# Kernel optimization log

Measured on AMD Instinct MI355X. Metric: run time of the kernel, lower is better.

## Reference

```python
import jax, jax.numpy as jnp
import numpy as np

E, D, H, F = 1024, 64, 16, 4096  # embedding, per-head dim, heads, mlp hidden
B, S = 2, 2048
EPS = 1e-5


def _layernorm(x, g, b):
    m = jnp.mean(x, axis=-1, keepdims=True)
    v = jnp.mean((x - m) ** 2, axis=-1, keepdims=True)
    return (x - m) * jax.lax.rsqrt(v + EPS) * g + b


def setup_inputs() -> dict:
    key = jax.random.key(0)
    ks = jax.random.split(key, 12)
    s_e = 1.0 / np.sqrt(E)
    s_f = 1.0 / np.sqrt(F)
    return {
        "x": jax.random.normal(ks[0], (B, S, E), jnp.float32),
        "Wq": jax.random.normal(ks[1], (H, E, D), jnp.float32) * s_e,
        "bq": jnp.zeros((H, D), jnp.float32),
        "Wk": jax.random.normal(ks[2], (H, E, D), jnp.float32) * s_e,
        "bk": jnp.zeros((H, D), jnp.float32),
        "Wv": jax.random.normal(ks[3], (H, E, D), jnp.float32) * s_e,
        "bv": jnp.zeros((H, D), jnp.float32),
        "Wo": jax.random.normal(ks[4], (E, E), jnp.float32) * s_e,
        "bo": jnp.zeros((E,), jnp.float32),
        "ln1_g": jnp.ones((E,), jnp.float32),
        "ln1_b": jnp.zeros((E,), jnp.float32),
        "ln2_g": jnp.ones((E,), jnp.float32),
        "ln2_b": jnp.zeros((E,), jnp.float32),
        "W1": jax.random.normal(ks[5], (E, F), jnp.float32) * s_e,
        "b1": jnp.zeros((F,), jnp.float32),
        "W2": jax.random.normal(ks[6], (F, E), jnp.float32) * s_f,
        "b2": jnp.zeros((E,), jnp.float32),
    }


def reference(x, Wq, bq, Wk, bk, Wv, bv, Wo, bo, ln1_g, ln1_b, ln2_g, ln2_b, W1, b1, W2, b2):
    h = _layernorm(x, ln1_g, ln1_b)
    # batched-head projections: [H,B,S,D]
    q = jnp.einsum("bse,hed->hbsd", h, Wq) + bq[:, None, None, :]
    k = jnp.einsum("bse,hed->hbsd", h, Wk) + bk[:, None, None, :]
    v = jnp.einsum("bse,hed->hbsd", h, Wv) + bv[:, None, None, :]
    # faithful quirk: scores = K @ Q^T (no 1/sqrt(d)), softmax over query axis
    scores = jnp.einsum("hbsd,hbtd->hbst", k, q)  # [H,B,S_key,S_query]
    att = jax.nn.softmax(scores, axis=-1)
    o = jnp.einsum("hbst,hbtd->hbsd", att, v)  # [H,B,S,D]
    o = jnp.transpose(o, (1, 2, 0, 3)).reshape(x.shape[0], x.shape[1], -1)  # concat heads
    x = x + o @ Wo + bo
    m = _layernorm(x, ln2_g, ln2_b)
    m = jax.nn.relu(m @ W1 + b1) @ W2 + b2
    return x + m
```

## Files before the change

### kernel.cpp

```cpp
#include <hip/hip_runtime.h>
#include <cstdint>
#include <cstddef>

typedef __attribute__((ext_vector_type(8))) short short8;
typedef __attribute__((ext_vector_type(4))) float f32x4;
typedef __attribute__((ext_vector_type(4))) unsigned short ushort4v;

#define E_DIM 1024
#define D_DIM 64
#define H_DIM 16
#define F_DIM 4096
#define B_DIM 2
#define S_DIM 2048
#define M_DIM 4096
#define LN_EPS 1e-5f
#define LOG2E 1.4426950408889634f

__device__ __forceinline__ float bf2f(unsigned short u) {
  union { unsigned int i; float f; } v;
  v.i = ((unsigned int)u) << 16;
  return v.f;
}
__device__ __forceinline__ unsigned short f2bf(float f) {
  union { float f; unsigned int i; } v;
  v.f = f;
  unsigned int r = v.i + 0x7FFFu + ((v.i >> 16) & 1u);
  return (unsigned short)(r >> 16);
}
__device__ __forceinline__ unsigned int cvt_pk_bf16(float a, float b) {
  unsigned int r;
  asm("v_cvt_pk_bf16_f32 %0, %1, %2" : "=v"(r) : "v"(a), "v"(b));
  return r;
}
__device__ __forceinline__ float exp2_fast(float x) {
  float r;
  asm("v_exp_f32 %0, %1" : "=v"(r) : "v"(x));
  return r;
}

__device__ __forceinline__ void gload_lds16(const unsigned short* src,
                                            unsigned short* dst) {
  __builtin_amdgcn_global_load_lds(
      (const __attribute__((address_space(1))) void*)src,
      (__attribute__((address_space(3))) void*)dst, 16, 0, 0);
}

template <bool QKV>
__global__ __launch_bounds__(256) void transpose_w(
    const float* __restrict__ in, unsigned short* __restrict__ ohi, int R,
    int C, float scale) {
  __shared__ float t[32][33];
  const int c0 = blockIdx.x * 32, r0 = blockIdx.y * 32;
  const int tid = threadIdx.x;
  {
    const int rr = tid >> 3, c4 = (tid & 7) * 4;
    size_t addr;
    if (QKV)
      addr = (size_t)(c0 >> 6) * 65536 + (size_t)(r0 + rr) * 64 +
             ((c0 & 63) + c4);
    else
      addr = (size_t)(r0 + rr) * C + (c0 + c4);
    float4 v = *(const float4*)(in + addr);
    t[rr][c4 + 0] = v.x;
    t[rr][c4 + 1] = v.y;
    t[rr][c4 + 2] = v.z;
    t[rr][c4 + 3] = v.w;
  }
  __syncthreads();
  {
    const int cc = tid >> 3, k4 = (tid & 7) * 4;
    ushort4v hi;
    hi.x = f2bf(t[k4 + 0][cc] * scale);
    hi.y = f2bf(t[k4 + 1][cc] * scale);
    hi.z = f2bf(t[k4 + 2][cc] * scale);
    hi.w = f2bf(t[k4 + 3][cc] * scale);
    *(ushort4v*)(ohi + (size_t)(c0 + cc) * R + (r0 + k4)) = hi;
  }
}

__global__ __launch_bounds__(256) void ln_kernel(const float* __restrict__ x,
                                                 const float* __restrict__ g,
                                                 const float* __restrict__ b,
                                                 unsigned short* __restrict__ o) {
  const int row = blockIdx.x;
  const float* xp = x + (size_t)row * E_DIM;
  const int t4 = threadIdx.x * 4;
  float4 xv = *(const float4*)(xp + t4);
  float s = xv.x + xv.y + xv.z + xv.w;
  float ss = xv.x * xv.x + xv.y * xv.y + xv.z * xv.z + xv.w * xv.w;
#pragma unroll
  for (int off = 32; off > 0; off >>= 1) {
    s += __shfl_down(s, off);
    ss += __shfl_down(ss, off);
  }
  __shared__ float red[8];
  const int wid = threadIdx.x >> 6;
  if ((threadIdx.x & 63) == 0) {
    red[wid] = s;
    red[4 + wid] = ss;
  }
  __syncthreads();
  if (threadIdx.x == 0) {
    float S = red[0] + red[1] + red[2] + red[3];
    float SS = red[4] + red[5] + red[6] + red[7];
    float mean = S * (1.0f / E_DIM);
    float var = SS * (1.0f / E_DIM) - mean * mean;
    red[0] = mean;
    red[1] = rsqrtf(var + LN_EPS);
  }
  __syncthreads();
  const float mean = red[0], rstd = red[1];
  float4 gv = *(const float4*)(g + t4);
  float4 bv = *(const float4*)(b + t4);
  ushort4v hi;
  hi.x = f2bf((xv.x - mean) * rstd * gv.x + bv.x);
  hi.y = f2bf((xv.y - mean) * rstd * gv.y + bv.y);
  hi.z = f2bf((xv.z - mean) * rstd * gv.z + bv.z);
  hi.w = f2bf((xv.w - mean) * rstd * gv.w + bv.w);
  *(ushort4v*)(o + (size_t)row * E_DIM + t4) = hi;
}

template <int MODE>
__global__ __launch_bounds__(256) void mfma_gemm(
    const unsigned short* __restrict__ A, const unsigned short* __restrict__ B,
    const float* __restrict__ bias, const float* __restrict__ bias2,
    const float* __restrict__ bias3, void* __restrict__ out0,
    void* __restrict__ out1, void* __restrict__ out2, int M, int N, int K) {
  __shared__ unsigned short As[8192];
  __shared__ unsigned short Bs[8192];
  const int tid = threadIdx.x;
  const int m0 = blockIdx.y * 128, n0 = blockIdx.x * 128;
  const int lane = tid & 63, wid = tid >> 6;
  const int wr = wid >> 1, wc = wid & 1;
  const int lr = lane & 15, lg = lane >> 4;

  f32x4 acc[4][4];
#pragma unroll
  for (int i = 0; i < 4; ++i)
#pragma unroll
    for (int j = 0; j < 4; ++j) acc[i][j] = {0.f, 0.f, 0.f, 0.f};

  int kbeg = 0, kend = K;
  if constexpr (MODE == 4) {
    int kslice = K / gridDim.z;
    kbeg = blockIdx.z * kslice;
    kend = kbeg + kslice;
  }

  for (int k0 = kbeg; k0 < kend; k0 += 64) {
#pragma unroll
    for (int c = 0; c < 4; ++c) {
      int chunk = wid * 4 + c;
      int rb = chunk >> 1, kc = chunk & 1;
      size_t goff = (size_t)(rb * 16 + lr) * K + k0 + kc * 32 + lg * 8;
      gload_lds16(A + (size_t)m0 * K + goff, As + chunk * 512);
      gload_lds16(B + (size_t)n0 * K + goff, Bs + chunk * 512);
    }
    __syncthreads();
#pragma unroll
    for (int kc = 0; kc < 2; ++kc) {
      short8 af[4], bf[4];
#pragma unroll
      for (int mi = 0; mi < 4; ++mi)
        af[mi] = *(const short8*)(As + ((wr * 4 + mi) * 2 + kc) * 512 + lane * 8);
#pragma unroll
      for (int ni = 0; ni < 4; ++ni)
        bf[ni] = *(const short8*)(Bs + ((wc * 4 + ni) * 2 + kc) * 512 + lane * 8);
      __builtin_amdgcn_s_setprio(1);
#pragma unroll
      for (int mi = 0; mi < 4; ++mi)
#pragma unroll
        for (int ni = 0; ni < 4; ++ni)
          acc[mi][ni] = __builtin_amdgcn_mfma_f32_16x16x32_bf16(
              af[mi], bf[ni], acc[mi][ni], 0, 0, 0);
      __builtin_amdgcn_s_setprio(0);
    }
    __syncthreads();
  }
#pragma unroll
  for (int mi = 0; mi < 4; ++mi) {
#pragma unroll
    for (int ni = 0; ni < 4; ++ni) {
      int n = n0 + wc * 64 + ni * 16 + lr;
#pragma unroll
      for (int rr = 0; rr < 4; ++rr) {
        int m = m0 + wr * 64 + mi * 16 + lg * 4 + rr;
        float v = acc[mi][ni][rr];
        if constexpr (MODE == 0) {
          int seg = n >> 10, nn = n & 1023;
          const float* bp = seg == 0 ? bias : seg == 1 ? bias2 : bias3;
          v += (seg == 0) ? bp[nn] * LOG2E : bp[nn];
          int hh = nn >> 6, d = nn & 63, bb = m >> 11, srow = m & 2047;
          size_t pb = (size_t)(hh * 2 + bb) * 131072;
          if (seg == 0)
            ((unsigned short*)out0)[pb + (size_t)srow * 64 + d] = f2bf(v);
          else if (seg == 1)
            ((unsigned short*)out1)[pb + (size_t)srow * 64 + d] = f2bf(v);
          else
            ((unsigned short*)out2)[pb + (size_t)d * 2048 + srow] = f2bf(v);
        } else if constexpr (MODE == 3) {
          ((unsigned short*)out0)[(size_t)m * N + n] = f2bf(fmaxf(v + bias[n], 0.f));
        } else {
          unsafeAtomicAdd((float*)out0 + (size_t)m * N + n, v);
        }
      }
    }
  }
}

__global__ __launch_bounds__(256, 4) void attn_mfma(
    const unsigned short* __restrict__ Q, const unsigned short* __restrict__ K,
    const unsigned short* __restrict__ Vt, unsigned short* __restrict__ O) {
  __shared__ unsigned short Qs[2][4096];
  __shared__ unsigned short Vs[2][4096];
  const int bid = blockIdx.x;
  const int wg = (bid & 7) * 128 + (bid >> 3);
  const int pair = wg >> 5, stile = wg & 31;
  const int tid = threadIdx.x, lane = tid & 63, wid = tid >> 6;
  const int lr = lane & 15, lg = lane >> 4;
  const size_t pbase = (size_t)pair * 131072;

  const int s_own = stile * 64 + wid * 16 + lr;
  short8 kb[2];
#pragma unroll
  for (int c = 0; c < 2; ++c)
    kb[c] = *(const short8*)(K + pbase + (size_t)s_own * 64 + c * 32 + lg * 8);

  f32x4 oa[4];
#pragma unroll
  for (int i = 0; i < 4; ++i) oa[i] = {0.f, 0.f, 0.f, 0.f};
  float mrun = -3e38f, lrun = 0.f;

  auto stage = [&](int buf, int t0) {
#pragma unroll
    for (int c = 0; c < 2; ++c) {
      int chunk = wid * 2 + c;
      gload_lds16(Q + pbase + (size_t)(t0 + wid * 16 + lr) * 64 + c * 32 + lg * 8,
                  &Qs[buf][chunk * 512]);
      gload_lds16(Vt + pbase + (size_t)(wid * 16 + lr) * 2048 + t0 + c * 32 + lg * 8,
                  &Vs[buf][chunk * 512]);
    }
  };

  stage(0, 0);
  __syncthreads();

  for (int it = 0; it < 32; ++it) {
    const int cur = it & 1;
    if (it < 31) stage(cur ^ 1, (it + 1) * 64);

    f32x4 sacc[4];
#pragma unroll
    for (int j = 0; j < 4; ++j) {
      sacc[j] = {0.f, 0.f, 0.f, 0.f};
      __builtin_amdgcn_s_setprio(1);
#pragma unroll
      for (int c = 0; c < 2; ++c) {
        short8 aq = *(const short8*)(&Qs[cur][(j * 2 + c) * 512 + lane * 8]);
        sacc[j] = __builtin_amdgcn_mfma_f32_16x16x32_bf16(aq, kb[c], sacc[j], 0, 0, 0);
      }
      __builtin_amdgcn_s_setprio(0);
    }
    float tm = fmaxf(
        fmaxf(fmaxf(fmaxf(sacc[0][0], sacc[0][1]), fmaxf(sacc[0][2], sacc[0][3])),
              fmaxf(fmaxf(sacc[1][0], sacc[1][1]), fmaxf(sacc[1][2], sacc[1][3]))),
        fmaxf(fmaxf(fmaxf(sacc[2][0], sacc[2][1]), fmaxf(sacc[2][2], sacc[2][3])),
              fmaxf(fmaxf(sacc[3][0], sacc[3][1]), fmaxf(sacc[3][2], sacc[3][3]))));
    tm = fmaxf(tm, __shfl_xor(tm, 16));
    tm = fmaxf(tm, __shfl_xor(tm, 32));
    if (!__all(tm - mrun <= 11.0f)) {
      float mnew = fmaxf(mrun, tm);
      float sc = exp2_fast(mrun - mnew);
      mrun = mnew;
      lrun *= sc;
#pragma unroll
      for (int di = 0; di < 4; ++di) {
        f32x4 t = oa[di];
        t[0] *= sc; t[1] *= sc; t[2] *= sc; t[3] *= sc;
        oa[di] = t;
      }
    }
    float p[4][4];
#pragma unroll
    for (int j = 0; j < 4; ++j)
#pragma unroll
      for (int r = 0; r < 4; ++r) p[j][r] = exp2_fast(sacc[j][r] - mrun);
    float lsum = ((p[0][0] + p[0][1]) + (p[0][2] + p[0][3])) +
                 ((p[1][0] + p[1][1]) + (p[1][2] + p[1][3])) +
                 ((p[2][0] + p[2][1]) + (p[2][2] + p[2][3])) +
                 ((p[3][0] + p[3][1]) + (p[3][2] + p[3][3]));
    lsum += __shfl_xor(lsum, 16);
    lsum += __shfl_xor(lsum, 32);
    lrun += lsum;
    unsigned int pw[4][2];
#pragma unroll
    for (int j = 0; j < 4; ++j) {
      pw[j][0] = cvt_pk_bf16(p[j][0], p[j][1]);
      pw[j][1] = cvt_pk_bf16(p[j][2], p[j][3]);
    }
#pragma unroll
    for (int kc = 0; kc < 2; ++kc) {
      unsigned int bw[4];
#pragma unroll
      for (int mm = 0; mm < 4; ++mm) {
        int src = ((lg & 1) * 2 + (mm >> 1)) * 16 + lr;
        int lo = __shfl((int)pw[2 * kc][mm & 1], src, 64);
        int hi = __shfl((int)pw[2 * kc + 1][mm & 1], src, 64);
        bw[mm] = (lg & 2) ? (unsigned)hi : (unsigned)lo;
      }
      union { unsigned int u[4]; short8 s8; } pb;
      pb.u[0] = bw[0]; pb.u[1] = bw[1]; pb.u[2] = bw[2]; pb.u[3] = bw[3];
      __builtin_amdgcn_s_setprio(1);
#pragma unroll
      for (int di = 0; di < 4; ++di) {
        short8 vf = *(const short8*)(&Vs[cur][(di * 2 + kc) * 512 + lane * 8]);
        oa[di] = __builtin_amdgcn_mfma_f32_16x16x32_bf16(vf, pb.s8, oa[di], 0, 0, 0);
      }
      __builtin_amdgcn_s_setprio(0);
    }
    __syncthreads();
  }

  const float inv = 1.f / lrun;
  const int b = pair & 1, h = pair >> 1;
  unsigned short* op = O + ((size_t)(b * 2048 + s_own)) * 1024 + h * 64;
#pragma unroll
  for (int di = 0; di < 4; ++di) {
    unsigned int w0 = cvt_pk_bf16(oa[di][0] * inv, oa[di][1] * inv);
    unsigned int w1 = cvt_pk_bf16(oa[di][2] * inv, oa[di][3] * inv);
    *(unsigned int*)(op + di * 16 + lg * 4) = w0;
    *(unsigned int*)(op + di * 16 + lg * 4 + 2) = w1;
  }
}

__global__ __launch_bounds__(256) void init_acc(const float* __restrict__ resid,
                                                const float* __restrict__ bias,
                                                float* __restrict__ out) {
  int i = blockIdx.x * 256 + threadIdx.x;
  float4 v = ((const float4*)resid)[i];
  float4 bb = ((const float4*)bias)[i & 255];
  v.x += bb.x; v.y += bb.y; v.z += bb.z; v.w += bb.w;
  ((float4*)out)[i] = v;
}

extern "C" void kernel_launch(void* const* d_in, const int* in_sizes, int n_in,
                              void* d_out, int out_size, void* d_ws,
                              size_t ws_size, hipStream_t stream) {
  const float* x = (const float*)d_in[0];
  const float* Wq = (const float*)d_in[1];
  const float* bq = (const float*)d_in[2];
  const float* Wk = (const float*)d_in[3];
  const float* bk = (const float*)d_in[4];
  const float* Wv = (const float*)d_in[5];
  const float* bv = (const float*)d_in[6];
  const float* Wo = (const float*)d_in[7];
  const float* bo = (const float*)d_in[8];
  const float* ln1_g = (const float*)d_in[9];
  const float* ln1_b = (const float*)d_in[10];
  const float* ln2_g = (const float*)d_in[11];
  const float* ln2_b = (const float*)d_in[12];
  const float* W1 = (const float*)d_in[13];
  const float* b1 = (const float*)d_in[14];
  const float* W2 = (const float*)d_in[15];
  const float* b2 = (const float*)d_in[16];

  char* w = (char*)d_ws;
  const size_t MB = 1024 * 1024;
  unsigned short* WqkvT = (unsigned short*)(w + 0 * MB);
  unsigned short* WoT = (unsigned short*)(w + 6 * MB);
  unsigned short* W1T = (unsigned short*)(w + 8 * MB);
  unsigned short* W2T = (unsigned short*)(w + 16 * MB);
  unsigned short* h = (unsigned short*)(w + 24 * MB);
  unsigned short* Qb = (unsigned short*)(w + 32 * MB);
  unsigned short* Kb = (unsigned short*)(w + 40 * MB);
  unsigned short* Vt = (unsigned short*)(w + 48 * MB);
  unsigned short* Obuf = (unsigned short*)(w + 56 * MB);
  unsigned short* m1 = (unsigned short*)(w + 32 * MB);
  float* x2 = (float*)(w + 64 * MB);

  const dim3 blk(256);

  transpose_w<true><<<dim3(32, 32), blk, 0, stream>>>(Wq, WqkvT, 1024, 1024, LOG2E);
  transpose_w<true><<<dim3(32, 32), blk, 0, stream>>>(Wk, WqkvT + 1048576, 1024, 1024, 1.f);
  transpose_w<true><<<dim3(32, 32), blk, 0, stream>>>(Wv, WqkvT + 2097152, 1024, 1024, 1.f);
  transpose_w<false><<<dim3(32, 32), blk, 0, stream>>>(Wo, WoT, 1024, 1024, 1.f);
  transpose_w<false><<<dim3(128, 32), blk, 0, stream>>>(W1, W1T, 1024, 4096, 1.f);
  transpose_w<false><<<dim3(32, 128), blk, 0, stream>>>(W2, W2T, 4096, 1024, 1.f);

  ln_kernel<<<M_DIM, blk, 0, stream>>>(x, ln1_g, ln1_b, h);

  mfma_gemm<0><<<dim3(24, 32), blk, 0, stream>>>(h, WqkvT, bq, bk, bv, Qb, Kb,
                                                 Vt, M_DIM, 3072, 1024);

  attn_mfma<<<1024, blk, 0, stream>>>(Qb, Kb, Vt, Obuf);

  init_acc<<<4096, blk, 0, stream>>>(x, bo, x2);
  mfma_gemm<4><<<dim3(8, 32, 2), blk, 0, stream>>>(Obuf, WoT, nullptr, nullptr,
                                                   nullptr, x2, nullptr,
                                                   nullptr, M_DIM, 1024, 1024);

  ln_kernel<<<M_DIM, blk, 0, stream>>>(x2, ln2_g, ln2_b, h);

  mfma_gemm<3><<<dim3(32, 32), blk, 0, stream>>>(h, W1T, b1, nullptr, nullptr,
                                                 m1, nullptr, nullptr, M_DIM,
                                                 4096, 1024);

  init_acc<<<4096, blk, 0, stream>>>(x2, b2, (float*)d_out);
  mfma_gemm<4><<<dim3(8, 32, 2), blk, 0, stream>>>(
      m1, W2T, nullptr, nullptr, nullptr, (float*)d_out, nullptr, nullptr,
      M_DIM, 1024, 4096);
}
```

Measured before the change: 494.2 us.

## Double-buffer GEMM LDS tiles, swizzle workgroups, fuse Wo residual epilogue

After: 500.9 us. Within noise of the previous version (+1.4%).

```diff
diff --git a/kernel.cpp b/kernel.cpp
--- a/kernel.cpp
+++ b/kernel.cpp
@@ -124,12 +124,16 @@
 __global__ __launch_bounds__(256) void mfma_gemm(
     const unsigned short* __restrict__ A, const unsigned short* __restrict__ B,
     const float* __restrict__ bias, const float* __restrict__ bias2,
-    const float* __restrict__ bias3, void* __restrict__ out0,
-    void* __restrict__ out1, void* __restrict__ out2, int M, int N, int K) {
-  __shared__ unsigned short As[8192];
-  __shared__ unsigned short Bs[8192];
+    const float* __restrict__ bias3, const float* __restrict__ resid,
+    void* __restrict__ out0, void* __restrict__ out1, void* __restrict__ out2,
+    int M, int N, int K) {
+  __shared__ unsigned short As[2][8192];
+  __shared__ unsigned short Bs[2][8192];
   const int tid = threadIdx.x;
-  const int m0 = blockIdx.y * 128, n0 = blockIdx.x * 128;
+  const int nwg = gridDim.x * gridDim.y;
+  const int flat = blockIdx.y * gridDim.x + blockIdx.x;
+  const int swz = (flat & 7) * (nwg >> 3) + (flat >> 3);
+  const int m0 = (swz / gridDim.x) * 128, n0 = (swz % gridDim.x) * 128;
   const int lane = tid & 63, wid = tid >> 6;
   const int wr = wid >> 1, wc = wid & 1;
   const int lr = lane & 15, lg = lane >> 4;
@@ -147,33 +151,39 @@
     kend = kbeg + kslice;
   }
 
-  for (int k0 = kbeg; k0 < kend; k0 += 64) {
+  auto stage = [&](int buf, int k0) {
 #pragma unroll
     for (int c = 0; c < 4; ++c) {
       int chunk = wid * 4 + c;
       int rb = chunk >> 1, kc = chunk & 1;
       size_t goff = (size_t)(rb * 16 + lr) * K + k0 + kc * 32 + lg * 8;
-      gload_lds16(A + (size_t)m0 * K + goff, As + chunk * 512);
-      gload_lds16(B + (size_t)n0 * K + goff, Bs + chunk * 512);
-    }
-    __syncthreads();
+      gload_lds16(A + (size_t)m0 * K + goff, &As[buf][chunk * 512]);
+      gload_lds16(B + (size_t)n0 * K + goff, &Bs[buf][chunk * 512]);
+    }
+  };
+
+  const int nt = (kend - kbeg) / 64;
+  stage(0, kbeg);
+  __syncthreads();
+
+  for (int it = 0; it < nt; ++it) {
+    const int cur = it & 1;
+    if (it + 1 < nt) stage(cur ^ 1, kbeg + (it + 1) * 64);
 #pragma unroll
     for (int kc = 0; kc < 2; ++kc) {
       short8 af[4], bf[4];
 #pragma unroll
       for (int mi = 0; mi < 4; ++mi)
-        af[mi] = *(const short8*)(As + ((wr * 4 + mi) * 2 + kc) * 512 + lane * 8);
+        af[mi] = *(const short8*)(&As[cur][((wr * 4 + mi) * 2 + kc) * 512 + lane * 8]);
 #pragma unroll
       for (int ni = 0; ni < 4; ++ni)
-        bf[ni] = *(const short8*)(Bs + ((wc * 4 + ni) * 2 + kc) * 512 + lane * 8);
-      __builtin_amdgcn_s_setprio(1);
+        bf[ni] = *(const short8*)(&Bs[cur][((wc * 4 + ni) * 2 + kc) * 512 + lane * 8]);
 #pragma unroll
       for (int mi = 0; mi < 4; ++mi)
 #pragma unroll
         for (int ni = 0; ni < 4; ++ni)
           acc[mi][ni] = __builtin_amdgcn_mfma_f32_16x16x32_bf16(
               af[mi], bf[ni], acc[mi][ni], 0, 0, 0);
-      __builtin_amdgcn_s_setprio(0);
     }
     __syncthreads();
   }
@@ -198,6 +208,9 @@
             ((unsigned short*)out1)[pb + (size_t)srow * 64 + d] = f2bf(v);
           else
             ((unsigned short*)out2)[pb + (size_t)d * 2048 + srow] = f2bf(v);
+        } else if constexpr (MODE == 2) {
+          size_t ad = (size_t)m * N + n;
+          ((float*)out0)[ad] = v + bias[n] + resid[ad];
         } else if constexpr (MODE == 3) {
           ((unsigned short*)out0)[(size_t)m * N + n] = f2bf(fmaxf(v + bias[n], 0.f));
         } else {
@@ -389,24 +402,23 @@
 
   ln_kernel<<<M_DIM, blk, 0, stream>>>(x, ln1_g, ln1_b, h);
 
-  mfma_gemm<0><<<dim3(24, 32), blk, 0, stream>>>(h, WqkvT, bq, bk, bv, Qb, Kb,
-                                                 Vt, M_DIM, 3072, 1024);
+  mfma_gemm<0><<<dim3(24, 32), blk, 0, stream>>>(h, WqkvT, bq, bk, bv, nullptr,
+                                                 Qb, Kb, Vt, M_DIM, 3072, 1024);
 
   attn_mfma<<<1024, blk, 0, stream>>>(Qb, Kb, Vt, Obuf);
 
-  init_acc<<<4096, blk, 0, stream>>>(x, bo, x2);
-  mfma_gemm<4><<<dim3(8, 32, 2), blk, 0, stream>>>(Obuf, WoT, nullptr, nullptr,
-                                                   nullptr, x2, nullptr,
-                                                   nullptr, M_DIM, 1024, 1024);
+  mfma_gemm<2><<<dim3(8, 32), blk, 0, stream>>>(Obuf, WoT, bo, nullptr, nullptr,
+                                                x, x2, nullptr, nullptr, M_DIM,
+                                                1024, 1024);
 
   ln_kernel<<<M_DIM, blk, 0, stream>>>(x2, ln2_g, ln2_b, h);
 
   mfma_gemm<3><<<dim3(32, 32), blk, 0, stream>>>(h, W1T, b1, nullptr, nullptr,
-                                                 m1, nullptr, nullptr, M_DIM,
-                                                 4096, 1024);
+                                                 nullptr, m1, nullptr, nullptr,
+                                                 M_DIM, 4096, 1024);
 
   init_acc<<<4096, blk, 0, stream>>>(x2, b2, (float*)d_out);
-  mfma_gemm<4><<<dim3(8, 32, 2), blk, 0, stream>>>(
-      m1, W2T, nullptr, nullptr, nullptr, (float*)d_out, nullptr, nullptr,
-      M_DIM, 1024, 4096);
-}
+  mfma_gemm<4><<<dim3(8, 32, 4), blk, 0, stream>>>(
+      m1, W2T, nullptr, nullptr, nullptr, nullptr, (float*)d_out, nullptr,
+      nullptr, M_DIM, 1024, 4096);
+}
```
